# Kernel tuning notes

Measured on AMD Instinct MI355X. Metric: run time of the kernel, lower is better.

## Reference

```python
import jax, jax.numpy as jnp
import numpy as np

N_NODES = 50000
N_FEAT = 128
N_HIDDEN = 256
N_CLASSES = 1
N_EDGES = 800000


def gcn_layer(x, src, dst, W, b, n_nodes):
    """GCNConv: D^-1/2 (A + I) D^-1/2 X W + b, via gather-scatter over edges."""
    h = x @ W  # [N, out]
    # add self loops
    loop = jnp.arange(n_nodes, dtype=src.dtype)
    s = jnp.concatenate([src, loop])
    d = jnp.concatenate([dst, loop])
    deg = jax.ops.segment_sum(jnp.ones_like(d, dtype=h.dtype), d, num_segments=n_nodes)
    inv_sqrt = jax.lax.rsqrt(jnp.maximum(deg, 1.0))
    norm = inv_sqrt[s] * inv_sqrt[d]  # [E+N]
    msgs = h[s] * norm[:, None]       # gather: [E+N, out]
    out = jax.ops.segment_sum(msgs, d, num_segments=n_nodes)  # scatter-add
    return out + b


def setup_inputs() -> dict:
    key = jax.random.key(0)
    k1, k2, k3, k4 = jax.random.split(key, 4)
    x = jax.random.normal(k1, (N_NODES, N_FEAT), dtype=jnp.float32)
    edge_index = jax.random.randint(k2, (2, N_EDGES), 0, N_NODES, dtype=jnp.int32)
    s1 = 1.0 / np.sqrt(N_FEAT)
    s2 = 1.0 / np.sqrt(N_HIDDEN)
    W1 = jax.random.uniform(k3, (N_FEAT, N_HIDDEN), jnp.float32, -s1, s1)
    b1 = jnp.zeros((N_HIDDEN,), jnp.float32)
    W2 = jax.random.uniform(k4, (N_HIDDEN, N_CLASSES), jnp.float32, -s2, s2)
    b2 = jnp.zeros((N_CLASSES,), jnp.float32)
    return {"x": x, "edge_index": edge_index, "W1": W1, "b1": b1, "W2": W2, "b2": b2}


def reference(x, edge_index, W1, b1, W2, b2):
    src, dst = edge_index[0], edge_index[1]
    n = x.shape[0]
    h = gcn_layer(x, src, dst, W1, b1, n)
    h = jax.nn.relu(h)  # dropout=0.0 -> identity
    out = gcn_layer(h, src, dst, W2, b2, n)
    return out  # [N, n_classes]
```

## Files before the change

kernel.cpp:

```cpp
#include <hip/hip_runtime.h>

typedef unsigned int uint;
typedef unsigned short ushort;
typedef __attribute__((ext_vector_type(2))) _Float16 h2;
typedef __attribute__((ext_vector_type(8))) _Float16 h8;
typedef __attribute__((ext_vector_type(4))) float f32x4;

#define CAP   64
#define BM16  16
#define STR   68
#define NPB   192
#define NBIN  261
#define CAPB  4096
#define EPB   4096

__device__ __forceinline__ uint pack_h2(float a, float b) {
  h2 v = {(_Float16)a, (_Float16)b};
  return __builtin_bit_cast(uint, v);
}

__global__ __launch_bounds__(1024) void k_part(
    const int* __restrict__ src, const int* __restrict__ dst,
    int* __restrict__ binCnt, uint* __restrict__ binData, int E,
    const float* __restrict__ W1, uint* __restrict__ wpack) {
  __shared__ int hist[NBIN];
  __shared__ int base[NBIN];
  int t = threadIdx.x;

  int gid = blockIdx.x * 1024 + t;
  if (gid < 4096) {
    int kk = gid >> 10, rem = gid & 1023, ntile = rem >> 6, ln = rem & 63;
    int quad = ln >> 4, nn = ntile * 16 + (ln & 15);
    uint w[4];
#pragma unroll
    for (int jp = 0; jp < 4; ++jp) {
      int k = kk * 32 + quad * 8 + 2 * jp;
      w[jp] = pack_h2(W1[k * 256 + nn], W1[(k + 1) * 256 + nn]);
    }
    *(uint4*)&wpack[gid * 4] = make_uint4(w[0], w[1], w[2], w[3]);
  }

  for (int i = t; i < NBIN; i += 1024) hist[i] = 0;
  __syncthreads();
  int s[4], d[4], b[4], r[4];
  bool v[4];
#pragma unroll
  for (int j = 0; j < 4; ++j) {
    int e = blockIdx.x * EPB + j * 1024 + t;
    v[j] = e < E;
    if (v[j]) {
      s[j] = src[e];
      d[j] = dst[e];
      b[j] = d[j] / NPB;
      r[j] = atomicAdd(&hist[b[j]], 1);
    }
  }
  __syncthreads();
  for (int i = t; i < NBIN; i += 1024) {
    int h = hist[i];
    base[i] = h ? atomicAdd(&binCnt[i], h) : 0;
  }
  __syncthreads();
#pragma unroll
  for (int j = 0; j < 4; ++j) {
    if (v[j]) {
      int idx = base[b[j]] + r[j];
      if (idx < CAPB)
        binData[b[j] * CAPB + idx] = (uint)s[j] | ((uint)d[j] << 16);
    }
  }
}

__global__ __launch_bounds__(1024) void k_bucketize(
    const uint* __restrict__ binData, const int* __restrict__ binCnt,
    ushort* __restrict__ col, int* __restrict__ cnt, int N,
    const float2* __restrict__ x2, uint* __restrict__ xs, float* __restrict__ inv) {
  __shared__ ushort col_l[NPB * CAP];
  __shared__ int cnt_l[NPB];
  int b = blockIdx.x, t = threadIdx.x;
  int lo = b * NPB;
  for (int i = t; i < NPB; i += 1024) cnt_l[i] = 0;
  uint* clz = (uint*)col_l;
  for (int i = t; i < NPB * (CAP / 2); i += 1024) clz[i] = 0;
  __syncthreads();
  int m = min(binCnt[b], CAPB);
  const uint* bd = &binData[b * CAPB];
  for (int e = t; e < m; e += 1024) {
    uint pr = bd[e];
    int sv = pr & 0xffffu;
    int dl = (int)(pr >> 16) - lo;
    int p = atomicAdd(&cnt_l[dl], 1);
    if (p < CAP) col_l[dl * CAP + p] = (ushort)sv;
  }
  __syncthreads();
  int nh = min(NPB, N - lo);
  if (nh <= 0) return;
  for (int i = t; i < nh; i += 1024) {
    int c = cnt_l[i];
    cnt[lo + i] = c;
    inv[lo + i] = rsqrtf((float)(c + 1));
  }
  uint* cg = (uint*)(col + (size_t)lo * CAP);
  const uint* cl = (const uint*)col_l;
  int nu = nh * (CAP / 2);
  for (int i = t; i < nu; i += 1024) cg[i] = cl[i];
  int nc = nh << 6;
  const float2* xb = x2 + ((size_t)lo << 6);
  uint* xo = xs + ((size_t)lo << 6);
  for (int i = t; i < nc; i += 1024) {
    float iv = rsqrtf((float)(cnt_l[i >> 6] + 1));
    float2 f = xb[i];
    xo[i] = pack_h2(iv * f.x, iv * f.y);
  }
}

__global__ __launch_bounds__(256, 4) void k_agg_gemm(
    const uint* __restrict__ xs, const ushort* __restrict__ col,
    const int* __restrict__ cnt, const float* __restrict__ inv,
    const uint* __restrict__ wpack, const float* __restrict__ b1,
    const float* __restrict__ W2, float* __restrict__ cz, int N) {
  __shared__ uint As[BM16 * STR];
  __shared__ float red[64];
  int t = threadIdx.x, wave = t >> 6, lane = t & 63;
  int m0 = blockIdx.x * BM16;

  int e4[4], ce4[4];
  h2 ac[4];
  float invd[4];
#pragma unroll
  for (int r = 0; r < 4; ++r) {
    int node = m0 + wave * 4 + r;
    if (node < N) {
      uint pd = xs[(size_t)node * 64 + lane];
      ac[r] = __builtin_bit_cast(h2, pd);
      e4[r] = min(cnt[node], CAP);
      ce4[r] = (int)col[(size_t)node * CAP + lane];
      invd[r] = inv[node];
    } else {
      e4[r] = 0; ce4[r] = 0; invd[r] = 0.f;
      ac[r] = (h2){(_Float16)0.f, (_Float16)0.f};
    }
  }
  int emax = max(max(e4[0], e4[1]), max(e4[2], e4[3]));
  for (int p = 0; p < emax; p += 8) {
    uint pv[4][8];
#pragma unroll
    for (int r = 0; r < 4; ++r) {
      if (p < e4[r]) {
#pragma unroll
        for (int j = 0; j < 8; ++j) {
          int s = __builtin_amdgcn_readlane(ce4[r], p + j);
          pv[r][j] = xs[(size_t)s * 64 + lane];
        }
      }
    }
#pragma unroll
    for (int r = 0; r < 4; ++r) {
      if (p < e4[r]) {
        int lim = e4[r] - p;
#pragma unroll
        for (int j = 0; j < 8; ++j) {
          uint u = (j < lim) ? pv[r][j] : 0u;
          ac[r] += __builtin_bit_cast(h2, u);
        }
      }
    }
  }
#pragma unroll
  for (int r = 0; r < 4; ++r) {
    _Float16 iv = (_Float16)invd[r];
    h2 aa = ac[r] * (h2){iv, iv};
    As[(wave * 4 + r) * STR + lane] = __builtin_bit_cast(uint, aa);
  }
  __syncthreads();

  int quad = lane >> 4, mrow = lane & 15;
  f32x4 acc[4];
#pragma unroll
  for (int nt = 0; nt < 4; ++nt) acc[nt] = (f32x4){0.f, 0.f, 0.f, 0.f};
#pragma unroll
  for (int kk = 0; kk < 4; ++kk) {
    h8 af = *(const h8*)&As[mrow * STR + kk * 16 + quad * 4];
#pragma unroll
    for (int nt = 0; nt < 4; ++nt) {
      int ntile = wave * 4 + nt;
      h8 bf = *(const h8*)&wpack[((kk * 16 + ntile) * 64 + lane) * 4];
      acc[nt] = __builtin_amdgcn_mfma_f32_16x16x32_f16(af, bf, acc[nt], 0, 0, 0);
    }
  }

  float partial[4] = {0.f, 0.f, 0.f, 0.f};
#pragma unroll
  for (int nt = 0; nt < 4; ++nt) {
    int c = (wave * 4 + nt) * 16 + mrow;
    float b1c = b1[c], w2c = W2[c];
#pragma unroll
    for (int r = 0; r < 4; ++r) {
      float h = fmaxf(acc[nt][r] + b1c, 0.f);
      partial[r] = fmaf(h, w2c, partial[r]);
    }
  }
#pragma unroll
  for (int r = 0; r < 4; ++r) {
    float p = partial[r];
    p += __shfl_xor(p, 1); p += __shfl_xor(p, 2);
    p += __shfl_xor(p, 4); p += __shfl_xor(p, 8);
    if (mrow == 0) red[wave * 16 + quad * 4 + r] = p;
  }
  __syncthreads();
  if (t < 16) {
    int node = m0 + t;
    if (node < N) {
      float s = red[t] + red[16 + t] + red[32 + t] + red[48 + t];
      cz[node] = inv[node] * s;
    }
  }
}

__global__ void k_agg2(const ushort* __restrict__ col, const int* __restrict__ cnt,
                       const float* __restrict__ cz, const float* __restrict__ b2,
                       float* __restrict__ out, int N) {
  int g = blockIdx.x * blockDim.x + threadIdx.x;
  int node = g >> 2, q = g & 3;
  if (node >= N) return;
  int e = min(cnt[node], CAP);
  float acc = (q == 0) ? cz[node] : 0.f;
  const ushort* cp = &col[node * CAP];
  for (int p = q; p < e; p += 4) acc += cz[cp[p]];
  acc += __shfl_xor(acc, 1);
  acc += __shfl_xor(acc, 2);
  if (q == 0) out[node] = rsqrtf((float)(cnt[node] + 1)) * acc + b2[0];
}

extern "C" void kernel_launch(void* const* d_in, const int* in_sizes, int n_in,
                              void* d_out, int out_size, void* d_ws, size_t ws_size,
                              hipStream_t stream) {
  const float2* x2 = (const float2*)d_in[0];
  const int*    ei = (const int*)d_in[1];
  const float*  W1 = (const float*)d_in[2];
  const float*  b1 = (const float*)d_in[3];
  const float*  W2 = (const float*)d_in[4];
  const float*  b2 = (const float*)d_in[5];
  int N = in_sizes[0] / 128;
  int E = in_sizes[1] / 2;
  const int* src = ei;
  const int* dst = ei + E;
  float* out = (float*)d_out;

  char* w = (char*)d_ws;
  size_t o = 0;
  auto carve = [&](size_t bytes) { char* p = w + o; o += (bytes + 255) & ~(size_t)255; return p; };
  int*    binCnt  = (int*)   carve((size_t)NBIN * 4);
  int*    cnt     = (int*)   carve((size_t)N * 4);
  uint*   binData = (uint*)  carve((size_t)NBIN * CAPB * 4);
  ushort* col     = (ushort*)carve((size_t)N * CAP * 2);
  uint*   xs      = (uint*)  carve((size_t)N * 64 * 4);
  float*  inv     = (float*) carve((size_t)N * 4);
  uint*   wpack   = (uint*)  carve(16384 * 4);
  float*  cz      = (float*) carve((size_t)N * 4);

  hipMemsetAsync(binCnt, 0, (size_t)NBIN * sizeof(int), stream);

  int nblk_p = (E + EPB - 1) / EPB;
  k_part<<<nblk_p, 1024, 0, stream>>>(src, dst, binCnt, binData, E, W1, wpack);

  k_bucketize<<<NBIN, 1024, 0, stream>>>(binData, binCnt, col, cnt, N, x2, xs, inv);

  k_agg_gemm<<<(N + BM16 - 1) / BM16, 256, 0, stream>>>(
      xs, col, cnt, inv, wpack, b1, W2, cz, N);

  long long tot2 = (long long)N * 4;
  k_agg2<<<(int)((tot2 + 255) / 256), 256, 0, stream>>>(col, cnt, cz, b2, out, N);
}
```

Measured before the change: 141.9 us.

## Fuse partition, bucketize, aggregation-GEMM and second aggregation into one cooperative kernel

Replaces the four separate launches with a single cooperative kernel of 224 blocks of 1024 threads, separating phases with grid-wide syncs. Each block owns one destination bin, so its per-node neighbour lists and degree counts stay in LDS across phases. The global col, cnt and inv arrays and their round trips are removed, and the inverse square roots are recomputed from the LDS counts. The intent is to remove launch gaps and intermediate global traffic. In exchange, the whole grid is pinned to one 16-wave block per CU during the latency-bound gather phase, and grid-sync overheads are added.

```diff
diff --git a/kernel.cpp b/kernel.cpp
--- a/kernel.cpp
+++ b/kernel.cpp
@@ -1,4 +1,7 @@
 #include <hip/hip_runtime.h>
+#include <hip/hip_cooperative_groups.h>
+
+namespace cg = cooperative_groups;
 
 typedef unsigned int uint;
 typedef unsigned short ushort;
@@ -7,27 +10,38 @@
 typedef __attribute__((ext_vector_type(4))) float f32x4;
 
 #define CAP   64
-#define BM16  16
+#define NPB   224
+#define NBIN  224
+#define NTILE 14
 #define STR   68
-#define NPB   192
-#define NBIN  261
 #define CAPB  4096
-#define EPB   4096
 
 __device__ __forceinline__ uint pack_h2(float a, float b) {
   h2 v = {(_Float16)a, (_Float16)b};
   return __builtin_bit_cast(uint, v);
 }
 
-__global__ __launch_bounds__(1024) void k_part(
+__global__ __launch_bounds__(1024) void k_fused(
     const int* __restrict__ src, const int* __restrict__ dst,
-    int* __restrict__ binCnt, uint* __restrict__ binData, int E,
-    const float* __restrict__ W1, uint* __restrict__ wpack) {
+    int* __restrict__ binCnt, uint* __restrict__ binData,
+    const float2* __restrict__ x2, uint* __restrict__ xs,
+    const float* __restrict__ W1, uint* __restrict__ wpack,
+    const float* __restrict__ b1, const float* __restrict__ W2,
+    const float* __restrict__ b2v, float* __restrict__ cz,
+    float* __restrict__ out, int N, int E, int EPB) {
+  __shared__ ushort col_l[NPB * CAP];
+  __shared__ int cnt_l[NPB];
   __shared__ int hist[NBIN];
   __shared__ int base[NBIN];
-  int t = threadIdx.x;
-
-  int gid = blockIdx.x * 1024 + t;
+  __shared__ uint As[4 * 16 * STR];
+  __shared__ float red[4 * 64];
+
+  cg::grid_group grid = cg::this_grid();
+  int b = blockIdx.x, t = threadIdx.x;
+  int lo = b * NPB;
+  int nh = min(NPB, N - lo);
+
+  int gid = b * 1024 + t;
   if (gid < 4096) {
     int kk = gid >> 10, rem = gid & 1023, ntile = rem >> 6, ln = rem & 63;
     int quad = ln >> 4, nn = ntile * 16 + (ln & 15);
@@ -42,17 +56,18 @@
 
   for (int i = t; i < NBIN; i += 1024) hist[i] = 0;
   __syncthreads();
-  int s[4], d[4], b[4], r[4];
-  bool v[4];
+  int base_e = b * EPB, end_e = min(E, base_e + EPB);
+  int s4[4], d4[4], bb[4], r4[4];
+  bool v4[4];
 #pragma unroll
   for (int j = 0; j < 4; ++j) {
-    int e = blockIdx.x * EPB + j * 1024 + t;
-    v[j] = e < E;
-    if (v[j]) {
-      s[j] = src[e];
-      d[j] = dst[e];
-      b[j] = d[j] / NPB;
-      r[j] = atomicAdd(&hist[b[j]], 1);
+    int e = base_e + j * 1024 + t;
+    v4[j] = e < end_e;
+    if (v4[j]) {
+      s4[j] = src[e];
+      d4[j] = dst[e];
+      bb[j] = d4[j] / NPB;
+      r4[j] = atomicAdd(&hist[bb[j]], 1);
     }
   }
   __syncthreads();
@@ -63,28 +78,21 @@
   __syncthreads();
 #pragma unroll
   for (int j = 0; j < 4; ++j) {
-    if (v[j]) {
-      int idx = base[b[j]] + r[j];
+    if (v4[j]) {
+      int idx = base[bb[j]] + r4[j];
       if (idx < CAPB)
-        binData[b[j] * CAPB + idx] = (uint)s[j] | ((uint)d[j] << 16);
-    }
-  }
-}
-
-__global__ __launch_bounds__(1024) void k_bucketize(
-    const uint* __restrict__ binData, const int* __restrict__ binCnt,
-    ushort* __restrict__ col, int* __restrict__ cnt, int N,
-    const float2* __restrict__ x2, uint* __restrict__ xs, float* __restrict__ inv) {
-  __shared__ ushort col_l[NPB * CAP];
-  __shared__ int cnt_l[NPB];
-  int b = blockIdx.x, t = threadIdx.x;
-  int lo = b * NPB;
+        binData[bb[j] * CAPB + idx] = (uint)s4[j] | ((uint)d4[j] << 16);
+    }
+  }
+  __threadfence();
+  grid.sync();
+
   for (int i = t; i < NPB; i += 1024) cnt_l[i] = 0;
   uint* clz = (uint*)col_l;
   for (int i = t; i < NPB * (CAP / 2); i += 1024) clz[i] = 0;
   __syncthreads();
   int m = min(binCnt[b], CAPB);
-  const uint* bd = &binData[b * CAPB];
+  const uint* bd = &binData[(size_t)b * CAPB];
   for (int e = t; e < m; e += 1024) {
     uint pr = bd[e];
     int sv = pr & 0xffffu;
@@ -93,17 +101,6 @@
     if (p < CAP) col_l[dl * CAP + p] = (ushort)sv;
   }
   __syncthreads();
-  int nh = min(NPB, N - lo);
-  if (nh <= 0) return;
-  for (int i = t; i < nh; i += 1024) {
-    int c = cnt_l[i];
-    cnt[lo + i] = c;
-    inv[lo + i] = rsqrtf((float)(c + 1));
-  }
-  uint* cg = (uint*)(col + (size_t)lo * CAP);
-  const uint* cl = (const uint*)col_l;
-  int nu = nh * (CAP / 2);
-  for (int i = t; i < nu; i += 1024) cg[i] = cl[i];
   int nc = nh << 6;
   const float2* xb = x2 + ((size_t)lo << 6);
   uint* xo = xs + ((size_t)lo << 6);
@@ -112,124 +109,125 @@
     float2 f = xb[i];
     xo[i] = pack_h2(iv * f.x, iv * f.y);
   }
-}
-
-__global__ __launch_bounds__(256, 4) void k_agg_gemm(
-    const uint* __restrict__ xs, const ushort* __restrict__ col,
-    const int* __restrict__ cnt, const float* __restrict__ inv,
-    const uint* __restrict__ wpack, const float* __restrict__ b1,
-    const float* __restrict__ W2, float* __restrict__ cz, int N) {
-  __shared__ uint As[BM16 * STR];
-  __shared__ float red[64];
-  int t = threadIdx.x, wave = t >> 6, lane = t & 63;
-  int m0 = blockIdx.x * BM16;
-
-  int e4[4], ce4[4];
-  h2 ac[4];
-  float invd[4];
-#pragma unroll
-  for (int r = 0; r < 4; ++r) {
-    int node = m0 + wave * 4 + r;
-    if (node < N) {
-      uint pd = xs[(size_t)node * 64 + lane];
-      ac[r] = __builtin_bit_cast(h2, pd);
-      e4[r] = min(cnt[node], CAP);
-      ce4[r] = (int)col[(size_t)node * CAP + lane];
-      invd[r] = inv[node];
-    } else {
-      e4[r] = 0; ce4[r] = 0; invd[r] = 0.f;
-      ac[r] = (h2){(_Float16)0.f, (_Float16)0.f};
-    }
-  }
-  int emax = max(max(e4[0], e4[1]), max(e4[2], e4[3]));
-  for (int p = 0; p < emax; p += 8) {
-    uint pv[4][8];
-#pragma unroll
-    for (int r = 0; r < 4; ++r) {
-      if (p < e4[r]) {
-#pragma unroll
-        for (int j = 0; j < 8; ++j) {
-          int s = __builtin_amdgcn_readlane(ce4[r], p + j);
-          pv[r][j] = xs[(size_t)s * 64 + lane];
-        }
-      }
-    }
-#pragma unroll
-    for (int r = 0; r < 4; ++r) {
-      if (p < e4[r]) {
-        int lim = e4[r] - p;
-#pragma unroll
-        for (int j = 0; j < 8; ++j) {
-          uint u = (j < lim) ? pv[r][j] : 0u;
-          ac[r] += __builtin_bit_cast(h2, u);
-        }
-      }
-    }
-  }
-#pragma unroll
-  for (int r = 0; r < 4; ++r) {
-    _Float16 iv = (_Float16)invd[r];
-    h2 aa = ac[r] * (h2){iv, iv};
-    As[(wave * 4 + r) * STR + lane] = __builtin_bit_cast(uint, aa);
-  }
-  __syncthreads();
-
+  __threadfence();
+  grid.sync();
+
+  int wave = t >> 6, lane = t & 63;
+  int wg = wave & 3, g = wave >> 2;
   int quad = lane >> 4, mrow = lane & 15;
-  f32x4 acc[4];
-#pragma unroll
-  for (int nt = 0; nt < 4; ++nt) acc[nt] = (f32x4){0.f, 0.f, 0.f, 0.f};
-#pragma unroll
-  for (int kk = 0; kk < 4; ++kk) {
-    h8 af = *(const h8*)&As[mrow * STR + kk * 16 + quad * 4];
-#pragma unroll
-    for (int nt = 0; nt < 4; ++nt) {
-      int ntile = wave * 4 + nt;
-      h8 bf = *(const h8*)&wpack[((kk * 16 + ntile) * 64 + lane) * 4];
-      acc[nt] = __builtin_amdgcn_mfma_f32_16x16x32_f16(af, bf, acc[nt], 0, 0, 0);
-    }
-  }
-
-  float partial[4] = {0.f, 0.f, 0.f, 0.f};
-#pragma unroll
-  for (int nt = 0; nt < 4; ++nt) {
-    int c = (wave * 4 + nt) * 16 + mrow;
-    float b1c = b1[c], w2c = W2[c];
-#pragma unroll
-    for (int r = 0; r < 4; ++r) {
-      float h = fmaxf(acc[nt][r] + b1c, 0.f);
-      partial[r] = fmaf(h, w2c, partial[r]);
-    }
-  }
-#pragma unroll
-  for (int r = 0; r < 4; ++r) {
-    float p = partial[r];
-    p += __shfl_xor(p, 1); p += __shfl_xor(p, 2);
-    p += __shfl_xor(p, 4); p += __shfl_xor(p, 8);
-    if (mrow == 0) red[wave * 16 + quad * 4 + r] = p;
-  }
-  __syncthreads();
-  if (t < 16) {
-    int node = m0 + t;
-    if (node < N) {
-      float s = red[t] + red[16 + t] + red[32 + t] + red[48 + t];
-      cz[node] = inv[node] * s;
-    }
-  }
-}
-
-__global__ void k_agg2(const ushort* __restrict__ col, const int* __restrict__ cnt,
-                       const float* __restrict__ cz, const float* __restrict__ b2,
-                       float* __restrict__ out, int N) {
-  int g = blockIdx.x * blockDim.x + threadIdx.x;
-  int node = g >> 2, q = g & 3;
-  if (node >= N) return;
-  int e = min(cnt[node], CAP);
-  float acc = (q == 0) ? cz[node] : 0.f;
-  const ushort* cp = &col[node * CAP];
-  for (int p = q; p < e; p += 4) acc += cz[cp[p]];
-  acc += __shfl_xor(acc, 1);
-  acc += __shfl_xor(acc, 2);
-  if (q == 0) out[node] = rsqrtf((float)(cnt[node] + 1)) * acc + b2[0];
+  for (int tt = 0; tt < 4; ++tt) {
+    int T = tt * 4 + g;
+    bool act = (T < NTILE);
+    int m0 = T * 16;
+    if (act) {
+      int e4[4], ce4[4];
+      h2 ac[4];
+#pragma unroll
+      for (int r = 0; r < 4; ++r) {
+        int nl = m0 + wg * 4 + r;
+        if (nl < nh) {
+          int c = cnt_l[nl];
+          e4[r] = min(c, CAP);
+          ce4[r] = (int)col_l[nl * CAP + lane];
+          ac[r] = __builtin_bit_cast(h2, xs[((size_t)(lo + nl)) * 64 + lane]);
+        } else {
+          e4[r] = 0; ce4[r] = 0;
+          ac[r] = (h2){(_Float16)0.f, (_Float16)0.f};
+        }
+      }
+      int emax = max(max(e4[0], e4[1]), max(e4[2], e4[3]));
+      for (int p = 0; p < emax; p += 8) {
+        uint pv[4][8];
+#pragma unroll
+        for (int r = 0; r < 4; ++r) {
+          if (p < e4[r]) {
+#pragma unroll
+            for (int j = 0; j < 8; ++j) {
+              int s = __builtin_amdgcn_readlane(ce4[r], p + j);
+              pv[r][j] = xs[(size_t)s * 64 + lane];
+            }
+          }
+        }
+#pragma unroll
+        for (int r = 0; r < 4; ++r) {
+          if (p < e4[r]) {
+            int lim = e4[r] - p;
+#pragma unroll
+            for (int j = 0; j < 8; ++j) {
+              uint u = (j < lim) ? pv[r][j] : 0u;
+              ac[r] += __builtin_bit_cast(h2, u);
+            }
+          }
+        }
+      }
+#pragma unroll
+      for (int r = 0; r < 4; ++r) {
+        int nl = m0 + wg * 4 + r;
+        float ivf = (nl < nh) ? rsqrtf((float)(cnt_l[nl] + 1)) : 0.f;
+        _Float16 iv = (_Float16)ivf;
+        h2 aa = ac[r] * (h2){iv, iv};
+        As[(g * 16 + wg * 4 + r) * STR + lane] = __builtin_bit_cast(uint, aa);
+      }
+    }
+    __syncthreads();
+    if (act) {
+      f32x4 acc[4];
+#pragma unroll
+      for (int nt = 0; nt < 4; ++nt) acc[nt] = (f32x4){0.f, 0.f, 0.f, 0.f};
+#pragma unroll
+      for (int kk = 0; kk < 4; ++kk) {
+        h8 af = *(const h8*)&As[(g * 16 + mrow) * STR + kk * 16 + quad * 4];
+#pragma unroll
+        for (int nt = 0; nt < 4; ++nt) {
+          int ntile = wg * 4 + nt;
+          h8 bf = *(const h8*)&wpack[((kk * 16 + ntile) * 64 + lane) * 4];
+          acc[nt] = __builtin_amdgcn_mfma_f32_16x16x32_f16(af, bf, acc[nt], 0, 0, 0);
+        }
+      }
+      float partial[4] = {0.f, 0.f, 0.f, 0.f};
+#pragma unroll
+      for (int nt = 0; nt < 4; ++nt) {
+        int c = (wg * 4 + nt) * 16 + mrow;
+        float b1c = b1[c], w2c = W2[c];
+#pragma unroll
+        for (int r = 0; r < 4; ++r) {
+          float h = fmaxf(acc[nt][r] + b1c, 0.f);
+          partial[r] = fmaf(h, w2c, partial[r]);
+        }
+      }
+#pragma unroll
+      for (int r = 0; r < 4; ++r) {
+        float p = partial[r];
+        p += __shfl_xor(p, 1); p += __shfl_xor(p, 2);
+        p += __shfl_xor(p, 4); p += __shfl_xor(p, 8);
+        if (mrow == 0) red[g * 64 + wg * 16 + quad * 4 + r] = p;
+      }
+    }
+    __syncthreads();
+    if (act && wg == 0 && lane < 16) {
+      int nl = m0 + lane;
+      if (nl < nh) {
+        float s = red[g * 64 + lane] + red[g * 64 + 16 + lane] +
+                  red[g * 64 + 32 + lane] + red[g * 64 + 48 + lane];
+        cz[lo + nl] = rsqrtf((float)(cnt_l[nl] + 1)) * s;
+      }
+    }
+  }
+  __threadfence();
+  grid.sync();
+
+  if (t < NPB * 4) {
+    int n = t >> 2, q = t & 3;
+    if (n < nh) {
+      int c = cnt_l[n];
+      int e = min(c, CAP);
+      float acc = (q == 0) ? cz[lo + n] : 0.f;
+      for (int p = q; p < e; p += 4) acc += cz[col_l[n * CAP + p]];
+      acc += __shfl_xor(acc, 1);
+      acc += __shfl_xor(acc, 2);
+      if (q == 0) out[lo + n] = rsqrtf((float)(c + 1)) * acc + b2v[0];
+    }
+  }
 }
 
 extern "C" void kernel_launch(void* const* d_in, const int* in_sizes, int n_in,
@@ -251,24 +249,19 @@
   size_t o = 0;
   auto carve = [&](size_t bytes) { char* p = w + o; o += (bytes + 255) & ~(size_t)255; return p; };
   int*    binCnt  = (int*)   carve((size_t)NBIN * 4);
-  int*    cnt     = (int*)   carve((size_t)N * 4);
   uint*   binData = (uint*)  carve((size_t)NBIN * CAPB * 4);
-  ushort* col     = (ushort*)carve((size_t)N * CAP * 2);
   uint*   xs      = (uint*)  carve((size_t)N * 64 * 4);
-  float*  inv     = (float*) carve((size_t)N * 4);
   uint*   wpack   = (uint*)  carve(16384 * 4);
   float*  cz      = (float*) carve((size_t)N * 4);
 
   hipMemsetAsync(binCnt, 0, (size_t)NBIN * sizeof(int), stream);
 
-  int nblk_p = (E + EPB - 1) / EPB;
-  k_part<<<nblk_p, 1024, 0, stream>>>(src, dst, binCnt, binData, E, W1, wpack);
-
-  k_bucketize<<<NBIN, 1024, 0, stream>>>(binData, binCnt, col, cnt, N, x2, xs, inv);
-
-  k_agg_gemm<<<(N + BM16 - 1) / BM16, 256, 0, stream>>>(
-      xs, col, cnt, inv, wpack, b1, W2, cz, N);
-
-  long long tot2 = (long long)N * 4;
-  k_agg2<<<(int)((tot2 + 255) / 256), 256, 0, stream>>>(col, cnt, cz, b2, out, N);
+  int EPB = (E + NBIN - 1) / NBIN;
+
+  void* args[] = {(void*)&src, (void*)&dst, (void*)&binCnt, (void*)&binData,
+                  (void*)&x2, (void*)&xs, (void*)&W1, (void*)&wpack,
+                  (void*)&b1, (void*)&W2, (void*)&b2, (void*)&cz,
+                  (void*)&out, (void*)&N, (void*)&E, (void*)&EPB};
+  hipLaunchCooperativeKernel((const void*)k_fused, dim3(NBIN), dim3(1024),
+                             args, 0, stream);
 }
```

Result: slower. 468.5 us (+230.1%).

## Replace two-pass binned CSR build with direct global atomics and fold normalization into gather

Applied to the files above, without the earlier changes.

Removes the bucketize kernel and the bin staging buffer. The partition kernel now builds the per-node adjacency directly with global atomicAdd on cnt and also converts x to fp16 without degree scaling. Source-side normalization moves into the aggregation kernel, where each lane computes rsqrt of its neighbour's degree and readlane broadcasts it per edge, and inv is recomputed from cnt instead of being stored. This saves one launch and a pass over x, at the cost of contended global atomics, scattered col writes, an extra cnt gather, and more fp16 multiplies in the inner loop.

```diff
diff --git a/kernel.cpp b/kernel.cpp
--- a/kernel.cpp
+++ b/kernel.cpp
@@ -9,10 +9,8 @@
 #define CAP   64
 #define BM16  16
 #define STR   68
-#define NPB   192
-#define NBIN  261
-#define CAPB  4096
 #define EPB   4096
+#define NBLK_PART 196
 
 __device__ __forceinline__ uint pack_h2(float a, float b) {
   h2 v = {(_Float16)a, (_Float16)b};
@@ -21,13 +19,12 @@
 
 __global__ __launch_bounds__(1024) void k_part(
     const int* __restrict__ src, const int* __restrict__ dst,
-    int* __restrict__ binCnt, uint* __restrict__ binData, int E,
-    const float* __restrict__ W1, uint* __restrict__ wpack) {
-  __shared__ int hist[NBIN];
-  __shared__ int base[NBIN];
+    int* __restrict__ cnt, ushort* __restrict__ col,
+    const float2* __restrict__ x2, uint* __restrict__ xr,
+    const float* __restrict__ W1, uint* __restrict__ wpack, int N, int E) {
   int t = threadIdx.x;
-
   int gid = blockIdx.x * 1024 + t;
+
   if (gid < 4096) {
     int kk = gid >> 10, rem = gid & 1023, ntile = rem >> 6, ln = rem & 63;
     int quad = ln >> 4, nn = ntile * 16 + (ln & 15);
@@ -40,104 +37,54 @@
     *(uint4*)&wpack[gid * 4] = make_uint4(w[0], w[1], w[2], w[3]);
   }
 
-  for (int i = t; i < NBIN; i += 1024) hist[i] = 0;
-  __syncthreads();
-  int s[4], d[4], b[4], r[4];
-  bool v[4];
 #pragma unroll
   for (int j = 0; j < 4; ++j) {
     int e = blockIdx.x * EPB + j * 1024 + t;
-    v[j] = e < E;
-    if (v[j]) {
-      s[j] = src[e];
-      d[j] = dst[e];
-      b[j] = d[j] / NPB;
-      r[j] = atomicAdd(&hist[b[j]], 1);
-    }
-  }
-  __syncthreads();
-  for (int i = t; i < NBIN; i += 1024) {
-    int h = hist[i];
-    base[i] = h ? atomicAdd(&binCnt[i], h) : 0;
-  }
-  __syncthreads();
-#pragma unroll
-  for (int j = 0; j < 4; ++j) {
-    if (v[j]) {
-      int idx = base[b[j]] + r[j];
-      if (idx < CAPB)
-        binData[b[j] * CAPB + idx] = (uint)s[j] | ((uint)d[j] << 16);
-    }
-  }
-}
-
-__global__ __launch_bounds__(1024) void k_bucketize(
-    const uint* __restrict__ binData, const int* __restrict__ binCnt,
-    ushort* __restrict__ col, int* __restrict__ cnt, int N,
-    const float2* __restrict__ x2, uint* __restrict__ xs, float* __restrict__ inv) {
-  __shared__ ushort col_l[NPB * CAP];
-  __shared__ int cnt_l[NPB];
-  int b = blockIdx.x, t = threadIdx.x;
-  int lo = b * NPB;
-  for (int i = t; i < NPB; i += 1024) cnt_l[i] = 0;
-  uint* clz = (uint*)col_l;
-  for (int i = t; i < NPB * (CAP / 2); i += 1024) clz[i] = 0;
-  __syncthreads();
-  int m = min(binCnt[b], CAPB);
-  const uint* bd = &binData[b * CAPB];
-  for (int e = t; e < m; e += 1024) {
-    uint pr = bd[e];
-    int sv = pr & 0xffffu;
-    int dl = (int)(pr >> 16) - lo;
-    int p = atomicAdd(&cnt_l[dl], 1);
-    if (p < CAP) col_l[dl * CAP + p] = (ushort)sv;
-  }
-  __syncthreads();
-  int nh = min(NPB, N - lo);
-  if (nh <= 0) return;
-  for (int i = t; i < nh; i += 1024) {
-    int c = cnt_l[i];
-    cnt[lo + i] = c;
-    inv[lo + i] = rsqrtf((float)(c + 1));
-  }
-  uint* cg = (uint*)(col + (size_t)lo * CAP);
-  const uint* cl = (const uint*)col_l;
-  int nu = nh * (CAP / 2);
-  for (int i = t; i < nu; i += 1024) cg[i] = cl[i];
-  int nc = nh << 6;
-  const float2* xb = x2 + ((size_t)lo << 6);
-  uint* xo = xs + ((size_t)lo << 6);
-  for (int i = t; i < nc; i += 1024) {
-    float iv = rsqrtf((float)(cnt_l[i >> 6] + 1));
-    float2 f = xb[i];
-    xo[i] = pack_h2(iv * f.x, iv * f.y);
+    if (e < E) {
+      int s = src[e], d = dst[e];
+      int p = atomicAdd(&cnt[d], 1);
+      if (p < CAP) col[(size_t)d * CAP + p] = (ushort)s;
+    }
+  }
+
+  int tot = N * 64;
+  for (int i = gid; i < tot; i += NBLK_PART * 1024) {
+    float2 f = x2[i];
+    xr[i] = pack_h2(f.x, f.y);
   }
 }
 
 __global__ __launch_bounds__(256, 4) void k_agg_gemm(
-    const uint* __restrict__ xs, const ushort* __restrict__ col,
-    const int* __restrict__ cnt, const float* __restrict__ inv,
-    const uint* __restrict__ wpack, const float* __restrict__ b1,
-    const float* __restrict__ W2, float* __restrict__ cz, int N) {
+    const uint* __restrict__ xr, const ushort* __restrict__ col,
+    const int* __restrict__ cnt, const uint* __restrict__ wpack,
+    const float* __restrict__ b1, const float* __restrict__ W2,
+    float* __restrict__ cz, int N) {
   __shared__ uint As[BM16 * STR];
   __shared__ float red[64];
   int t = threadIdx.x, wave = t >> 6, lane = t & 63;
   int m0 = blockIdx.x * BM16;
 
   int e4[4], ce4[4];
+  uint ivu4[4];
   h2 ac[4];
   float invd[4];
 #pragma unroll
   for (int r = 0; r < 4; ++r) {
     int node = m0 + wave * 4 + r;
     if (node < N) {
-      uint pd = xs[(size_t)node * 64 + lane];
-      ac[r] = __builtin_bit_cast(h2, pd);
-      e4[r] = min(cnt[node], CAP);
-      ce4[r] = (int)col[(size_t)node * CAP + lane];
-      invd[r] = inv[node];
+      int c = cnt[node];
+      e4[r] = min(c, CAP);
+      invd[r] = rsqrtf((float)(c + 1));
+      int ce = (int)col[(size_t)node * CAP + lane];
+      ce4[r] = ce;
+      float ivs = (lane < e4[r]) ? rsqrtf((float)(cnt[ce] + 1)) : 0.f;
+      ushort hb = __builtin_bit_cast(ushort, (_Float16)ivs);
+      ivu4[r] = (uint)hb | ((uint)hb << 16);
+      uint u = xr[(size_t)node * 64 + lane];
+      _Float16 ivh = (_Float16)invd[r];
+      ac[r] = __builtin_bit_cast(h2, u) * (h2){ivh, ivh};
     } else {
-      e4[r] = 0; ce4[r] = 0; invd[r] = 0.f;
+      e4[r] = 0; ce4[r] = 0; ivu4[r] = 0; invd[r] = 0.f;
       ac[r] = (h2){(_Float16)0.f, (_Float16)0.f};
     }
   }
@@ -150,7 +97,7 @@
 #pragma unroll
         for (int j = 0; j < 8; ++j) {
           int s = __builtin_amdgcn_readlane(ce4[r], p + j);
-          pv[r][j] = xs[(size_t)s * 64 + lane];
+          pv[r][j] = xr[(size_t)s * 64 + lane];
         }
       }
     }
@@ -160,17 +107,18 @@
         int lim = e4[r] - p;
 #pragma unroll
         for (int j = 0; j < 8; ++j) {
+          uint ivp = (uint)__builtin_amdgcn_readlane((int)ivu4[r], p + j);
           uint u = (j < lim) ? pv[r][j] : 0u;
-          ac[r] += __builtin_bit_cast(h2, u);
+          ac[r] += __builtin_bit_cast(h2, u) * __builtin_bit_cast(h2, ivp);
         }
       }
     }
   }
 #pragma unroll
   for (int r = 0; r < 4; ++r) {
-    _Float16 iv = (_Float16)invd[r];
-    h2 aa = ac[r] * (h2){iv, iv};
-    As[(wave * 4 + r) * STR + lane] = __builtin_bit_cast(uint, aa);
+    float ax = invd[r] * (float)ac[r].x;
+    float ay = invd[r] * (float)ac[r].y;
+    As[(wave * 4 + r) * STR + lane] = pack_h2(ax, ay);
   }
   __syncthreads();
 
@@ -212,7 +160,7 @@
     int node = m0 + t;
     if (node < N) {
       float s = red[t] + red[16 + t] + red[32 + t] + red[48 + t];
-      cz[node] = inv[node] * s;
+      cz[node] = rsqrtf((float)(cnt[node] + 1)) * s;
     }
   }
 }
@@ -225,7 +173,8 @@
   if (node >= N) return;
   int e = min(cnt[node], CAP);
   float acc = (q == 0) ? cz[node] : 0.f;
-  const ushort* cp = &col[node * CAP];
+  const ushort* cp = &col[(size_t)node * CAP];
+#pragma unroll 4
   for (int p = q; p < e; p += 4) acc += cz[cp[p]];
   acc += __shfl_xor(acc, 1);
   acc += __shfl_xor(acc, 2);
@@ -250,24 +199,21 @@
   char* w = (char*)d_ws;
   size_t o = 0;
   auto carve = [&](size_t bytes) { char* p = w + o; o += (bytes + 255) & ~(size_t)255; return p; };
-  int*    binCnt  = (int*)   carve((size_t)NBIN * 4);
-  int*    cnt     = (int*)   carve((size_t)N * 4);
-  uint*   binData = (uint*)  carve((size_t)NBIN * CAPB * 4);
-  ushort* col     = (ushort*)carve((size_t)N * CAP * 2);
-  uint*   xs      = (uint*)  carve((size_t)N * 64 * 4);
-  float*  inv     = (float*) carve((size_t)N * 4);
-  uint*   wpack   = (uint*)  carve(16384 * 4);
-  float*  cz      = (float*) carve((size_t)N * 4);
-
-  hipMemsetAsync(binCnt, 0, (size_t)NBIN * sizeof(int), stream);
+  int*    cnt   = (int*)   carve((size_t)N * 4);
+  ushort* col   = (ushort*)carve((size_t)N * CAP * 2);
+  uint*   xr    = (uint*)  carve((size_t)N * 64 * 4);
+  char*   pad   =          carve((size_t)4352 * 1024);
+  uint*   wpack = (uint*)  carve(16384 * 4);
+  float*  cz    = (float*) carve((size_t)N * 4);
+  (void)pad;
+
+  hipMemsetAsync(cnt, 0, (size_t)N * sizeof(int), stream);
 
   int nblk_p = (E + EPB - 1) / EPB;
-  k_part<<<nblk_p, 1024, 0, stream>>>(src, dst, binCnt, binData, E, W1, wpack);
-
-  k_bucketize<<<NBIN, 1024, 0, stream>>>(binData, binCnt, col, cnt, N, x2, xs, inv);
+  k_part<<<nblk_p, 1024, 0, stream>>>(src, dst, cnt, col, x2, xr, W1, wpack, N, E);
 
   k_agg_gemm<<<(N + BM16 - 1) / BM16, 256, 0, stream>>>(
-      xs, col, cnt, inv, wpack, b1, W2, cz, N);
+      xr, col, cnt, wpack, b1, W2, cz, N);
 
   long long tot2 = (long long)N * 4;
   k_agg2<<<(int)((tot2 + 255) / 256), 256, 0, stream>>>(col, cnt, cz, b2, out, N);
```

New measurement: 173.7 us. +22.4%, slower.
